# Kernel tuning notes

Hardware: AMD Instinct MI355X
Metric: run time of the kernel (lower is better)

Reference implementation:

```python
import jax, jax.numpy as jnp
import numpy as np

N, DIN, DOUT = 8192, 2048, 2048


def setup_inputs() -> dict:
    key = jax.random.key(0)
    k1, k2, k3 = jax.random.split(key, 3)
    x = jax.random.normal(k1, (N, DIN), dtype=jnp.float32)
    # quantized params: uint8 kernel, uint16 bias (as produced by model.quantize)
    qkernel = jax.random.randint(k2, (DIN, DOUT), 0, 256, dtype=jnp.int32).astype(jnp.uint8)
    qbias = jax.random.randint(k3, (DOUT,), 0, 65536, dtype=jnp.int32).astype(jnp.uint16)
    scale = jnp.array(0.5, dtype=jnp.float32)
    zero_point = jnp.array(0.5, dtype=jnp.float32)
    return {"x": x, "scale": scale, "zero_point": zero_point,
            "qkernel": qkernel, "qbias": qbias}


def reference(x, scale, zero_point, qkernel, qbias) -> jnp.ndarray:
    # quantize(x, b=8, uint8): clip(round(x/scale) + zero_point, 0, 255)
    qmax = 2 ** 8 - 1
    xq = jnp.clip(jnp.round(x / scale) + zero_point, 0, qmax).astype(jnp.uint8)
    acc = jnp.dot(xq, qkernel, preferred_element_type=jnp.uint16)
    acc = (acc + qbias).astype(jnp.uint32)  # uint16 add wraps, then widen
    # dequantize: (x - zero_point) * scale  -> float32
    return (acc - zero_point) * scale
```

## Files before the change

kernel.cpp:

```cpp
#include <hip/hip_runtime.h>
#include <stdint.h>


#define NROWS 8192
#define DIN   2048
#define DOUT  2048

typedef int v4i __attribute__((ext_vector_type(4)));

__device__ inline void gload16(const uint8_t* g, uint8_t* l) {
  __builtin_amdgcn_global_load_lds(
      (__attribute__((address_space(1))) void*)(g),
      (__attribute__((address_space(3))) void*)(l), 16, 0, 0);
}

__device__ inline void wgbar() {
  __builtin_amdgcn_sched_barrier(0);
  __builtin_amdgcn_s_barrier();
  __builtin_amdgcn_sched_barrier(0);
}

__device__ inline uint32_t q4(float4 v, float inv, float z, int& sum) {
  uint32_t w = 0;
  float e[4] = {v.x, v.y, v.z, v.w};
#pragma unroll
  for (int i = 0; i < 4; ++i) {
    float tq = rintf(e[i] * inv) + z;
    tq = fminf(fmaxf(tq, 0.0f), 255.0f);
    uint32_t q = (uint32_t)tq;
    sum += (int)q;
    w |= ((q ^ 0x80u) & 0xFFu) << (8 * i);
  }
  return w;
}

__global__ __launch_bounds__(256) void kp(const float* __restrict__ x,
                                          const float* __restrict__ sp,
                                          const float* __restrict__ zpp,
                                          const void* __restrict__ qk,
                                          const void* __restrict__ qbias,
                                          uint8_t* __restrict__ xq,
                                          int* __restrict__ rs128,
                                          uint8_t* __restrict__ qkT,
                                          int* __restrict__ qb32) {
  const int t = threadIdx.x;
  if (blockIdx.x < NROWS) {
    const int row = blockIdx.x;
    const float s = sp[0], z = zpp[0];
    const float inv = 1.0f / s;
    const float4* xr = (const float4*)(x + (size_t)row * DIN);
    float4 a = xr[t];
    float4 b = xr[t + 256];
    int sum = 0;
    uint32_t w0 = q4(a, inv, z, sum);
    uint32_t w1 = q4(b, inv, z, sum);
    uint32_t* xw = (uint32_t*)(xq + (size_t)row * DIN);
    xw[t] = w0;
    xw[t + 256] = w1;
#pragma unroll
    for (int o = 32; o > 0; o >>= 1) sum += __shfl_down(sum, o);
    __shared__ int ws4[4];
    if ((t & 63) == 0) ws4[t >> 6] = sum;
    __syncthreads();
    if (t == 0) rs128[row] = 128 * (ws4[0] + ws4[1] + ws4[2] + ws4[3]);
    return;
  }
  __shared__ uint8_t tile[64][68];
  __shared__ int sflag;
  if (t == 0) sflag = 0;
  __syncthreads();
  {
    const int* q32 = (const int*)qk;
    int bad = 0;
#pragma unroll
    for (int i = 0; i < 4; ++i) bad |= ((unsigned)q32[t + 256 * i] > 255u);
    if (bad) sflag = 1;
  }
  __syncthreads();
  const int u8mode = sflag;

  const int j = blockIdx.x - NROWS;
  const int n0 = (j & 31) * 64;
  const int k0 = (j >> 5) * 64;
  const int tx = t & 15;
  const int ty = t >> 4;
  if (u8mode) {
    const uint8_t* q8 = (const uint8_t*)qk;
#pragma unroll
    for (int jj = 0; jj < 4; ++jj) {
      int r = jj * 16 + ty;
      uint32_t w = *(const uint32_t*)(q8 + (size_t)(k0 + r) * DOUT + n0 + tx * 4);
      tile[r][tx * 4 + 0] = (uint8_t)(w & 255u);
      tile[r][tx * 4 + 1] = (uint8_t)((w >> 8) & 255u);
      tile[r][tx * 4 + 2] = (uint8_t)((w >> 16) & 255u);
      tile[r][tx * 4 + 3] = (uint8_t)((w >> 24) & 255u);
    }
  } else {
    const int* q32 = (const int*)qk;
#pragma unroll
    for (int jj = 0; jj < 4; ++jj) {
      int r = jj * 16 + ty;
      int4 w = *(const int4*)(q32 + (size_t)(k0 + r) * DOUT + n0 + tx * 4);
      tile[r][tx * 4 + 0] = (uint8_t)w.x;
      tile[r][tx * 4 + 1] = (uint8_t)w.y;
      tile[r][tx * 4 + 2] = (uint8_t)w.z;
      tile[r][tx * 4 + 3] = (uint8_t)w.w;
    }
  }
  __syncthreads();
#pragma unroll
  for (int jj = 0; jj < 4; ++jj) {
    int r = jj * 16 + ty;
    uint32_t b0 = tile[tx * 4 + 0][r];
    uint32_t b1 = tile[tx * 4 + 1][r];
    uint32_t b2 = tile[tx * 4 + 2][r];
    uint32_t b3 = tile[tx * 4 + 3][r];
    *(uint32_t*)(qkT + (size_t)(n0 + r) * DIN + k0 + tx * 4) =
        (b0 ^ 0x80u) | ((b1 ^ 0x80u) << 8) | ((b2 ^ 0x80u) << 16) | ((b3 ^ 0x80u) << 24);
  }
  if (k0 == 0 && t < 64) {
    int n = n0 + t;
    qb32[n] = u8mode ? (int)((const uint16_t*)qbias)[n] : ((const int*)qbias)[n];
  }
}

__global__ __launch_bounds__(512, 2) void kg(const uint8_t* __restrict__ A,
                                             const uint8_t* __restrict__ B,
                                             const int* __restrict__ rs128,
                                             const int* __restrict__ qb32,
                                             const float* __restrict__ sp,
                                             const float* __restrict__ zpp,
                                             float* __restrict__ out) {
  __shared__ __align__(16) uint8_t lds[131072];
  const int t = threadIdx.x;
  const int l = t & 63, wid = t >> 6;
  const int wr = wid >> 2, wc = wid & 3;
  const int rl = l & 15, kgp = l >> 4;

  const int bid = blockIdx.x;
  const int swz = (bid & 7) * 32 + (bid >> 3);
  const int m0 = (swz >> 3) * 256;
  const int n0 = (swz & 7) * 256;

  const int srow = t >> 2;
  const int sc = (t & 3) ^ ((srow >> 1) & 3);
  const uint8_t* gA = A + (size_t)(m0 + srow) * DIN + sc * 16;
  const uint8_t* gA2 = gA + (size_t)128 * DIN;
  const uint8_t* gB = B + (size_t)(n0 + srow) * DIN + sc * 16;
  const uint8_t* gB2 = gB + (size_t)128 * DIN;
  const int sdst = t * 16;

#define STAGE_A(BUF, KS, KB) do {                                   \
    uint8_t* d_ = lds + (BUF) * 32768 + (KS) * 16384 + sdst;        \
    gload16(gA + (KB) + (KS) * 64, d_);                             \
    gload16(gA2 + (KB) + (KS) * 64, d_ + 8192);                     \
  } while (0)
#define STAGE_B(BUF, KS, KB) do {                                   \
    uint8_t* d_ = lds + 65536 + (BUF) * 32768 + (KS) * 16384 + sdst;\
    gload16(gB + (KB) + (KS) * 64, d_);                             \
    gload16(gB2 + (KB) + (KS) * 64, d_ + 8192);                     \
  } while (0)

  const int swl = (rl >> 1) & 3;
  const int aoff0 = (wr * 128 + rl) * 64 + ((kgp ^ swl) << 4);
  const int boff0 = 65536 + (wc * 64 + rl) * 64 + ((kgp ^ swl) << 4);

  v4i acc[8][4];
#pragma unroll
  for (int i = 0; i < 8; ++i)
#pragma unroll
    for (int j = 0; j < 4; ++j) acc[i][j] = (v4i){0, 0, 0, 0};
  v4i csum[4];
#pragma unroll
  for (int j = 0; j < 4; ++j) csum[j] = (v4i){0, 0, 0, 0};
  const v4i ones = (v4i){0x01010101, 0x01010101, 0x01010101, 0x01010101};
  v4i af[4], bf[4];

#define LD_A(MH, KH) do {                                            \
    const uint8_t* ap_ = lds + cur * 32768 + (KH) * 16384 + aoff0 + (MH) * 4096; \
    _Pragma("unroll")                                                \
    for (int q = 0; q < 4; ++q) af[q] = *(const v4i*)(ap_ + q * 1024);\
  } while (0)
#define LD_B(KH) do {                                                \
    const uint8_t* bp_ = lds + cur * 32768 + (KH) * 16384 + boff0;   \
    _Pragma("unroll")                                                \
    for (int nj = 0; nj < 4; ++nj) bf[nj] = *(const v4i*)(bp_ + nj * 1024); \
  } while (0)
#define DO_MFMA(MH) do {                                             \
    __builtin_amdgcn_s_setprio(1);                                   \
    _Pragma("unroll")                                                \
    for (int q = 0; q < 4; ++q)                                      \
      _Pragma("unroll")                                              \
      for (int nj = 0; nj < 4; ++nj)                                 \
        acc[(MH) * 4 + q][nj] = __builtin_amdgcn_mfma_i32_16x16x64_i8(\
            af[q], bf[nj], acc[(MH) * 4 + q][nj], 0, 0, 0);          \
    __builtin_amdgcn_s_setprio(0);                                   \
  } while (0)
#define DO_CSUM() do {                                               \
    _Pragma("unroll")                                                \
    for (int nj = 0; nj < 4; ++nj)                                   \
      csum[nj] = __builtin_amdgcn_mfma_i32_16x16x64_i8(              \
          ones, bf[nj], csum[nj], 0, 0, 0);                          \
  } while (0)

  STAGE_A(0, 0, 0);
  STAGE_B(0, 0, 0);
  STAGE_A(0, 1, 0);
  STAGE_B(0, 1, 0);

  int cur = 0;
  for (int tt = 0; tt < 16; ++tt) {
    const int nb = cur ^ 1;
    const int kn = ((tt + 1) & 15) * 128;
    asm volatile("s_waitcnt vmcnt(4)" ::: "memory");
    wgbar();
    LD_B(0);
    LD_A(0, 0);
    STAGE_A(nb, 0, kn);
    DO_MFMA(0);
    DO_CSUM();
    wgbar();
    LD_A(1, 0);
    STAGE_B(nb, 0, kn);
    DO_MFMA(1);
    asm volatile("s_waitcnt vmcnt(4)" ::: "memory");
    wgbar();
    LD_B(1);
    LD_A(0, 1);
    STAGE_A(nb, 1, kn);
    DO_MFMA(0);
    DO_CSUM();
    wgbar();
    LD_A(1, 1);
    STAGE_B(nb, 1, kn);
    DO_MFMA(1);
    cur = nb;
  }

  const float s = sp[0], z = zpp[0];
  int cc[4];
#pragma unroll
  for (int nj = 0; nj < 4; ++nj) cc[nj] = (csum[nj][0] << 7) + qb32[n0 + wc * 64 + nj * 16 + rl];
#pragma unroll
  for (int mi = 0; mi < 8; ++mi) {
#pragma unroll
    for (int r = 0; r < 4; ++r) {
      int row = m0 + wr * 128 + mi * 16 + kgp * 4 + r;
      int rs = rs128[row];
#pragma unroll
      for (int nj = 0; nj < 4; ++nj) {
        int col = n0 + wc * 64 + nj * 16 + rl;
        uint32_t v = (uint32_t)(acc[mi][nj][r] + rs + cc[nj]) & 0xFFFFu;
        out[(size_t)row * DOUT + col] = ((float)v - z) * s;
      }
    }
  }
#undef STAGE_A
#undef STAGE_B
#undef LD_A
#undef LD_B
#undef DO_MFMA
#undef DO_CSUM
}

extern "C" void kernel_launch(void* const* d_in, const int* in_sizes, int n_in,
                              void* d_out, int out_size, void* d_ws, size_t ws_size,
                              hipStream_t stream) {
  const float* x   = (const float*)d_in[0];
  const float* sp  = (const float*)d_in[1];
  const float* zpp = (const float*)d_in[2];
  const void*  qk  = d_in[3];
  const void*  qb  = d_in[4];
  float* out = (float*)d_out;

  uint8_t* ws = (uint8_t*)d_ws;
  uint8_t* xq  = ws;
  uint8_t* qkT = ws + (16u << 20);
  int* rs128 = (int*)(ws + (20u << 20));
  int* qb32  = (int*)(ws + (20u << 20) + (32u << 10));

  kp<<<NROWS + (DIN / 64) * (DOUT / 64), 256, 0, stream>>>(
      x, sp, zpp, qk, qb, xq, rs128, qkT, qb32);
  kg<<<dim3(256), 512, 0, stream>>>(xq, qkT, rs128, qb32, sp, zpp, out);
}
```

Baseline: 160.9 us.

## Restructure GEMM main loop into barrier-fenced load/MFMA clusters with explicit lgkm waits

Reorganizes each K-step into four phases. Each phase issues LDS fragment reads and global-to-LDS staging, passes a workgroup barrier, waits for lgkmcnt(0), then runs an MFMA cluster, with the column-sum MFMAs folded into the cluster. The vmcnt wait moves to the end of the iteration and a prologue wait is added. The aim is to keep the MFMA bursts across waves in lockstep, ping-pong style, so memory and compute phases interleave. The cost is twice as many barriers per iteration and full LDS drains before each cluster.

```diff
diff --git a/kernel.cpp b/kernel.cpp
--- a/kernel.cpp
+++ b/kernel.cpp
@@ -186,7 +186,11 @@
     _Pragma("unroll")                                                \
     for (int nj = 0; nj < 4; ++nj) bf[nj] = *(const v4i*)(bp_ + nj * 1024); \
   } while (0)
-#define DO_MFMA(MH) do {                                             \
+#define LGKM0() do {                                                 \
+    asm volatile("s_waitcnt lgkmcnt(0)" ::: "memory");               \
+    __builtin_amdgcn_sched_barrier(0);                               \
+  } while (0)
+#define CLUSTER(MH, CS) do {                                         \
     __builtin_amdgcn_s_setprio(1);                                   \
     _Pragma("unroll")                                                \
     for (int q = 0; q < 4; ++q)                                      \
@@ -194,46 +198,59 @@
       for (int nj = 0; nj < 4; ++nj)                                 \
         acc[(MH) * 4 + q][nj] = __builtin_amdgcn_mfma_i32_16x16x64_i8(\
             af[q], bf[nj], acc[(MH) * 4 + q][nj], 0, 0, 0);          \
+    if (CS) {                                                        \
+      _Pragma("unroll")                                              \
+      for (int nj = 0; nj < 4; ++nj)                                 \
+        csum[nj] = __builtin_amdgcn_mfma_i32_16x16x64_i8(            \
+            ones, bf[nj], csum[nj], 0, 0, 0);                        \
+    }                                                                \
     __builtin_amdgcn_s_setprio(0);                                   \
-  } while (0)
-#define DO_CSUM() do {                                               \
-    _Pragma("unroll")                                                \
-    for (int nj = 0; nj < 4; ++nj)                                   \
-      csum[nj] = __builtin_amdgcn_mfma_i32_16x16x64_i8(              \
-          ones, bf[nj], csum[nj], 0, 0, 0);                          \
   } while (0)
 
   STAGE_A(0, 0, 0);
   STAGE_B(0, 0, 0);
   STAGE_A(0, 1, 0);
   STAGE_B(0, 1, 0);
+  asm volatile("s_waitcnt vmcnt(4)" ::: "memory");
+  wgbar();
 
   int cur = 0;
   for (int tt = 0; tt < 16; ++tt) {
     const int nb = cur ^ 1;
     const int kn = ((tt + 1) & 15) * 128;
-    asm volatile("s_waitcnt vmcnt(4)" ::: "memory");
-    wgbar();
+
     LD_B(0);
     LD_A(0, 0);
     STAGE_A(nb, 0, kn);
-    DO_MFMA(0);
-    DO_CSUM();
-    wgbar();
+    wgbar();
+    LGKM0();
+    CLUSTER(0, 1);
+    wgbar();
+
     LD_A(1, 0);
     STAGE_B(nb, 0, kn);
-    DO_MFMA(1);
+    wgbar();
+    LGKM0();
+    CLUSTER(1, 0);
     asm volatile("s_waitcnt vmcnt(4)" ::: "memory");
     wgbar();
+
     LD_B(1);
     LD_A(0, 1);
     STAGE_A(nb, 1, kn);
-    DO_MFMA(0);
-    DO_CSUM();
-    wgbar();
+    wgbar();
+    LGKM0();
+    CLUSTER(0, 1);
+    wgbar();
+
     LD_A(1, 1);
     STAGE_B(nb, 1, kn);
-    DO_MFMA(1);
+    wgbar();
+    LGKM0();
+    CLUSTER(1, 0);
+    asm volatile("s_waitcnt vmcnt(4)" ::: "memory");
+    wgbar();
+
     cur = nb;
   }
 
@@ -259,8 +276,8 @@
 #undef STAGE_B
 #undef LD_A
 #undef LD_B
-#undef DO_MFMA
-#undef DO_CSUM
+#undef LGKM0
+#undef CLUSTER
 }
 
 extern "C" void kernel_launch(void* const* d_in, const int* in_sizes, int n_in,
```

Measured after the change: 162.6 us. Within noise of the previous version (+1.0%).

## Switch int8 GEMM to 32x32x32 MFMA tiles with reworked LDS schedule

Applied to the files above, without the earlier changes.

Replaces the 16x16x64 i8 MFMA tiling with 32x32x32 i8 MFMA, so each wave holds 4x2 accumulators of 16 ints instead of 8x4 of 4. The LDS fragment loads and the main loop are restructured into four k-substeps per tile, each with fused A/B loads, an MFMA cluster and a plain barrier, and the sched_barrier wrappers are dropped. The intent is fewer LDS reads per MFMA and fewer MFMA issues, which should raise throughput. The risk is that barrier placement without sched_barrier lets the compiler reorder work, and that the csum MFMA now runs every substep.

```diff
diff --git a/kernel.cpp b/kernel.cpp
--- a/kernel.cpp
+++ b/kernel.cpp
@@ -6,18 +6,13 @@
 #define DIN   2048
 #define DOUT  2048
 
-typedef int v4i __attribute__((ext_vector_type(4)));
+typedef int v4i  __attribute__((ext_vector_type(4)));
+typedef int v16i __attribute__((ext_vector_type(16)));
 
 __device__ inline void gload16(const uint8_t* g, uint8_t* l) {
   __builtin_amdgcn_global_load_lds(
       (__attribute__((address_space(1))) void*)(g),
       (__attribute__((address_space(3))) void*)(l), 16, 0, 0);
-}
-
-__device__ inline void wgbar() {
-  __builtin_amdgcn_sched_barrier(0);
-  __builtin_amdgcn_s_barrier();
-  __builtin_amdgcn_sched_barrier(0);
 }
 
 __device__ inline uint32_t q4(float4 v, float inv, float z, int& sum) {
@@ -135,7 +130,8 @@
   const int t = threadIdx.x;
   const int l = t & 63, wid = t >> 6;
   const int wr = wid >> 2, wc = wid & 3;
-  const int rl = l & 15, kgp = l >> 4;
+  const int rl = l & 31;
+  const int hk = l >> 5;
 
   const int bid = blockIdx.x;
   const int swz = (bid & 7) * 32 + (bid >> 3);
@@ -162,105 +158,107 @@
   } while (0)
 
   const int swl = (rl >> 1) & 3;
-  const int aoff0 = (wr * 128 + rl) * 64 + ((kgp ^ swl) << 4);
-  const int boff0 = 65536 + (wc * 64 + rl) * 64 + ((kgp ^ swl) << 4);
-
-  v4i acc[8][4];
-#pragma unroll
-  for (int i = 0; i < 8; ++i)
-#pragma unroll
-    for (int j = 0; j < 4; ++j) acc[i][j] = (v4i){0, 0, 0, 0};
-  v4i csum[4];
-#pragma unroll
-  for (int j = 0; j < 4; ++j) csum[j] = (v4i){0, 0, 0, 0};
+  const int cb = (hk ^ swl) << 4;
+  const int arow = (wr * 128 + rl) * 64;
+  const int brow = 65536 + (wc * 64 + rl) * 64;
+
+  v16i acc[4][2];
+#pragma unroll
+  for (int i = 0; i < 4; ++i)
+#pragma unroll
+    for (int j = 0; j < 2; ++j) acc[i][j] = (v16i)(0);
+  v16i csum[2];
+  csum[0] = (v16i)(0);
+  csum[1] = (v16i)(0);
   const v4i ones = (v4i){0x01010101, 0x01010101, 0x01010101, 0x01010101};
-  v4i af[4], bf[4];
-
-#define LD_A(MH, KH) do {                                            \
-    const uint8_t* ap_ = lds + cur * 32768 + (KH) * 16384 + aoff0 + (MH) * 4096; \
-    _Pragma("unroll")                                                \
-    for (int q = 0; q < 4; ++q) af[q] = *(const v4i*)(ap_ + q * 1024);\
-  } while (0)
-#define LD_B(KH) do {                                                \
-    const uint8_t* bp_ = lds + cur * 32768 + (KH) * 16384 + boff0;   \
-    _Pragma("unroll")                                                \
-    for (int nj = 0; nj < 4; ++nj) bf[nj] = *(const v4i*)(bp_ + nj * 1024); \
-  } while (0)
-#define DO_MFMA(MH) do {                                             \
+  v4i af[4], bf[2];
+
+#define LD_AB(S) do {                                                \
+    const int sl_ = cur * 32768 + ((S) >> 1) * 16384 +               \
+                    (cb ^ (((S) & 1) << 5));                         \
+    _Pragma("unroll")                                                \
+    for (int nt = 0; nt < 2; ++nt)                                   \
+      bf[nt] = *(const v4i*)(lds + sl_ + brow + nt * 2048);          \
+    _Pragma("unroll")                                                \
+    for (int mt = 0; mt < 4; ++mt)                                   \
+      af[mt] = *(const v4i*)(lds + sl_ + arow + mt * 2048);          \
+  } while (0)
+#define CLUSTER() do {                                               \
     __builtin_amdgcn_s_setprio(1);                                   \
     _Pragma("unroll")                                                \
-    for (int q = 0; q < 4; ++q)                                      \
+    for (int mt = 0; mt < 4; ++mt)                                   \
       _Pragma("unroll")                                              \
-      for (int nj = 0; nj < 4; ++nj)                                 \
-        acc[(MH) * 4 + q][nj] = __builtin_amdgcn_mfma_i32_16x16x64_i8(\
-            af[q], bf[nj], acc[(MH) * 4 + q][nj], 0, 0, 0);          \
+      for (int nt = 0; nt < 2; ++nt)                                 \
+        acc[mt][nt] = __builtin_amdgcn_mfma_i32_32x32x32_i8(         \
+            af[mt], bf[nt], acc[mt][nt], 0, 0, 0);                   \
+    _Pragma("unroll")                                                \
+    for (int nt = 0; nt < 2; ++nt)                                   \
+      csum[nt] = __builtin_amdgcn_mfma_i32_32x32x32_i8(              \
+          ones, bf[nt], csum[nt], 0, 0, 0);                          \
     __builtin_amdgcn_s_setprio(0);                                   \
-  } while (0)
-#define DO_CSUM() do {                                               \
-    _Pragma("unroll")                                                \
-    for (int nj = 0; nj < 4; ++nj)                                   \
-      csum[nj] = __builtin_amdgcn_mfma_i32_16x16x64_i8(              \
-          ones, bf[nj], csum[nj], 0, 0, 0);                          \
   } while (0)
 
   STAGE_A(0, 0, 0);
   STAGE_B(0, 0, 0);
   STAGE_A(0, 1, 0);
   STAGE_B(0, 1, 0);
+  asm volatile("s_waitcnt vmcnt(4)" ::: "memory");
+  __builtin_amdgcn_s_barrier();
 
   int cur = 0;
   for (int tt = 0; tt < 16; ++tt) {
     const int nb = cur ^ 1;
     const int kn = ((tt + 1) & 15) * 128;
+
+    LD_AB(0);
+    STAGE_A(nb, 0, kn);
+    CLUSTER();
+    __builtin_amdgcn_s_barrier();
+
+    LD_AB(1);
+    STAGE_B(nb, 0, kn);
+    CLUSTER();
     asm volatile("s_waitcnt vmcnt(4)" ::: "memory");
-    wgbar();
-    LD_B(0);
-    LD_A(0, 0);
-    STAGE_A(nb, 0, kn);
-    DO_MFMA(0);
-    DO_CSUM();
-    wgbar();
-    LD_A(1, 0);
-    STAGE_B(nb, 0, kn);
-    DO_MFMA(1);
+    __builtin_amdgcn_s_barrier();
+
+    LD_AB(2);
+    STAGE_A(nb, 1, kn);
+    CLUSTER();
+    __builtin_amdgcn_s_barrier();
+
+    LD_AB(3);
+    STAGE_B(nb, 1, kn);
+    CLUSTER();
     asm volatile("s_waitcnt vmcnt(4)" ::: "memory");
-    wgbar();
-    LD_B(1);
-    LD_A(0, 1);
-    STAGE_A(nb, 1, kn);
-    DO_MFMA(0);
-    DO_CSUM();
-    wgbar();
-    LD_A(1, 1);
-    STAGE_B(nb, 1, kn);
-    DO_MFMA(1);
+    __builtin_amdgcn_s_barrier();
+
     cur = nb;
   }
 
   const float s = sp[0], z = zpp[0];
-  int cc[4];
-#pragma unroll
-  for (int nj = 0; nj < 4; ++nj) cc[nj] = (csum[nj][0] << 7) + qb32[n0 + wc * 64 + nj * 16 + rl];
-#pragma unroll
-  for (int mi = 0; mi < 8; ++mi) {
-#pragma unroll
-    for (int r = 0; r < 4; ++r) {
-      int row = m0 + wr * 128 + mi * 16 + kgp * 4 + r;
+  int cc[2], col[2];
+#pragma unroll
+  for (int nt = 0; nt < 2; ++nt) {
+    col[nt] = n0 + wc * 64 + nt * 32 + rl;
+    cc[nt] = (csum[nt][0] << 7) + qb32[col[nt]];
+  }
+#pragma unroll
+  for (int mt = 0; mt < 4; ++mt) {
+#pragma unroll
+    for (int r = 0; r < 16; ++r) {
+      int row = m0 + wr * 128 + mt * 32 + (r & 3) + 8 * (r >> 2) + 4 * hk;
       int rs = rs128[row];
 #pragma unroll
-      for (int nj = 0; nj < 4; ++nj) {
-        int col = n0 + wc * 64 + nj * 16 + rl;
-        uint32_t v = (uint32_t)(acc[mi][nj][r] + rs + cc[nj]) & 0xFFFFu;
-        out[(size_t)row * DOUT + col] = ((float)v - z) * s;
+      for (int nt = 0; nt < 2; ++nt) {
+        uint32_t v = (uint32_t)(acc[mt][nt][r] + rs + cc[nt]) & 0xFFFFu;
+        out[(size_t)row * DOUT + col[nt]] = ((float)v - z) * s;
       }
     }
   }
 #undef STAGE_A
 #undef STAGE_B
-#undef LD_A
-#undef LD_B
-#undef DO_MFMA
-#undef DO_CSUM
+#undef LD_AB
+#undef CLUSTER
 }
 
 extern "C" void kernel_launch(void* const* d_in, const int* in_sizes, int n_in,
```

Measured after the change: 175.3 us. 1.09x slower.
